# Optimization experiments

Measured on AMD Instinct MI355X. Metric: run time of the kernel, lower is better.

## Reference

```python
import jax, jax.numpy as jnp
import numpy as np

B, S, H = 8, 2048, 1024   # batch, seq, hidden_size
E = 4                     # num_experts (world_size=1 -> all local)
C = 1024                  # kv_cache_size (cache_decrement=0 -> uniform pyramid)
R = 4                     # LoRA rank
ALPHA = 1.0
TOP_K = 2
TEMP = 1.0
KEEP = C // 2             # pyramid compressor keeps top-half by importance


def _lora(z, A, Bm):
    # LoRALayer: (z @ A) @ B scaled by alpha/rank
    return (z @ A) @ Bm * (ALPHA / A.shape[-1])


def setup_inputs() -> dict:
    key = jax.random.key(0)
    ks = jax.random.split(key, 24)
    w = lambda k, shp: jax.random.normal(k, shp, jnp.float32) * 0.02
    return {
        'x': jax.random.normal(ks[0], (B, S, H), jnp.float32),
        'query': jax.random.normal(ks[1], (B, S, H), jnp.float32),
        'Wg': w(ks[2], (H, E)), 'bg': jnp.zeros((E,), jnp.float32),
        'Wq': w(ks[3], (H, H)), 'bq': jnp.zeros((H,), jnp.float32),
        'Wk': w(ks[4], (H, H)), 'bk': jnp.zeros((H,), jnp.float32),
        'Aq': w(ks[5], (H, R)), 'Bq': w(ks[6], (R, H)),
        'Ak': w(ks[7], (H, R)), 'Bk': w(ks[8], (R, H)),
        'We': w(ks[9], (E, H, H)), 'be': jnp.zeros((E, H), jnp.float32),
        'Ae': w(ks[10], (E, H, R)), 'Be': w(ks[11], (E, R, H)),
        'Av': w(ks[12], (E, H, R)), 'Bv': w(ks[13], (E, R, H)),
        'cache_keys': jax.random.normal(ks[14], (E, C, H), jnp.float32),
        'cache_values': jax.random.normal(ks[15], (E, C, H), jnp.float32),
        'cache_imp': jax.random.uniform(ks[16], (E, C), jnp.float32),
    }


def reference(x, query, Wg, bg, Wq, bq, Wk, bk, Aq, Bq, Ak, Bk,
              We, be, Ae, Be, Av, Bv, cache_keys, cache_values, cache_imp):
    # ---- AdaptiveRouter: softmax gate, top-2 renormalized, load-balance loss ----
    probs = jax.nn.softmax((x @ Wg + bg) / TEMP, axis=-1)             # [B,S,E]
    tw, ti = jax.lax.top_k(probs, TOP_K)                              # [B,S,K]
    twn = tw / tw.sum(-1, keepdims=True)
    onehot = jax.nn.one_hot(ti, E, dtype=x.dtype)                     # [B,S,K,E]
    routing = jnp.einsum('bsk,bske->bse', twn, onehot)                # [B,S,E]
    lb_loss = E * jnp.sum(probs.mean((0, 1)) * onehot.mean((0, 1, 2)))

    # ---- compute_token_importance (query provided): LoRA-augmented q/k attention ----
    q = query @ Wq + bq + _lora(query, Aq, Bq)
    k = x @ Wk + bk + _lora(x, Ak, Bk)
    att = jax.nn.softmax(jnp.einsum('bqh,bkh->bqk', q, k) / np.sqrt(H).astype(np.float32), axis=-1)
    importance = att.sum(axis=1)                                      # [B,S] column sums

    # ---- per-expert LoRA forward + pyramid-compressed cache read ----
    def expert_fn(We_i, be_i, Ae_i, Be_i, Av_i, Bv_i, cv_i, ci_i):
        eo = x @ We_i + be_i + _lora(x, Ae_i, Be_i)                   # [B,S,H]
        idx = jax.lax.top_k(ci_i, KEEP)[1]                            # keep top-half by importance
        vals = cv_i[idx]                                              # [KEEP,H] irregular gather
        vals = vals + _lora(vals, Av_i, Bv_i)                         # value LoRA on compressed cache
        return eo + jax.lax.stop_gradient(vals.mean(0))               # cached values are detached

    outs = jax.vmap(expert_fn)(We, be, Ae, Be, Av, Bv, cache_values, cache_imp)  # [E,B,S,H]
    expert_output = jnp.einsum('ebsh,bse->bsh', outs, routing)

    # ---- cache update at ptr=0 (detached buffer mutation -> returned new state) ----
    sg = jax.lax.stop_gradient
    new_keys = cache_keys.at[:, 0].set(jnp.broadcast_to(sg(x.mean((0, 1))), (E, H)))
    new_values = cache_values.at[:, 0].set(sg(outs.mean((1, 2))))
    new_imp = cache_imp.at[:, 0].set(sg(importance.mean()))
    return expert_output, lb_loss, new_keys, new_values, new_imp
```

## Files before the change

kernel.cpp:

```cpp
#include <hip/hip_runtime.h>

constexpr int kH    = 1024;
constexpr int kNT   = 16384;
constexpr int kE    = 4;
constexpr int kC    = 1024;
constexpr int kR    = 4;
constexpr int kKeep = 512;
constexpr float kLoraScale = 0.25f;
constexpr int kCapTiles = 136;
constexpr int kCapRows  = kCapTiles * 128;
constexpr int kNB      = kNT / 256;

constexpr size_t WS_RW     = 0;
constexpr size_t WS_G      = 65536;
constexpr size_t WS_XSUM   = 393216;
constexpr size_t WS_SHADOW = 394240;
constexpr size_t WS_TU     = 394752;
constexpr size_t WS_VBAR   = 394784;
constexpr size_t WS_FX     = 398880;
constexpr size_t WS_NEWV0  = 402976;
constexpr size_t WS_MSK    = 407072;
constexpr size_t WS_GBASE  = 411168;
constexpr size_t WS_BHIST  = 411176;
constexpr size_t WS_BOFF   = 411560;
constexpr size_t WS_RTPID  = 411944;
constexpr size_t WS_TPID   = 412088;
constexpr size_t WS_GRO    = 428472;
constexpr size_t WS_PERM   = 444856;
constexpr size_t WS_WCAT   = 462264;
constexpr size_t WS_AEXT   = 482744;
constexpr size_t WS_AEXTG  = 744888;
constexpr size_t WS_BEXT   = 1023416;
constexpr size_t WS_WET    = 1039800;
constexpr size_t WS_XG     = 3136952;

constexpr size_t OUT_LB = 16777216;
constexpr size_t OUT_NK = 16777217;

typedef __attribute__((ext_vector_type(8))) short bf16x8;
typedef __attribute__((ext_vector_type(4))) float f32x4;

__device__ __forceinline__ float wred(float v) {
#pragma unroll
  for (int off = 32; off; off >>= 1) v += __shfl_xor(v, off);
  return v;
}

__device__ __forceinline__ ushort f2bf(float f) {
  unsigned int u = __float_as_uint(f);
  u += 0x7FFFu + ((u >> 16) & 1u);
  return (ushort)(u >> 16);
}

__device__ __forceinline__ void gload16(const ushort* g, ushort* l) {
  __builtin_amdgcn_global_load_lds(
      (const __attribute__((address_space(1))) unsigned int*)g,
      (__attribute__((address_space(3))) unsigned int*)l, 16, 0, 0);
}

__device__ __forceinline__ int pid_a(int pid) { return pid < 3 ? 0 : (pid < 5 ? 1 : 2); }
__device__ __forceinline__ int pid_b(int pid) { return pid < 3 ? pid + 1 : (pid < 5 ? pid - 1 : 3); }

__global__ __launch_bounds__(256) void wcat_k(const float* __restrict__ Wg,
                                              const float* __restrict__ Ae,
                                              float* __restrict__ wcat) {
  const int idx = blockIdx.x * 256 + threadIdx.x;
  const int c = idx >> 10, k = idx & 1023;
  float v;
  if (c < 4) v = Wg[(size_t)k * 4 + c];
  else {
    const int e = (c - 4) >> 2, r = (c - 4) & 3;
    v = Ae[((size_t)e * kH + k) * kR + r];
  }
  wcat[(size_t)c * kH + k] = v;
}

__global__ __launch_bounds__(256) void router_gemm_k(
    const float* __restrict__ x, const float* __restrict__ wcat,
    float* __restrict__ G) {
  __shared__ float xs_l[128][64];
  __shared__ float wt_l[20][64];
  const int tid = threadIdx.x;
  const int t0 = blockIdx.x * 128;
  const int tok = tid & 127, half = tid >> 7, cb = half * 10;
  float acc[10] = {};
  for (int kc = 0; kc < 16; ++kc) {
#pragma unroll
    for (int i = 0; i < 8; ++i) {
      const int idx = tid + i * 256;
      const int stok = idx >> 4, sslot = idx & 15;
      const float4 v =
          *(const float4*)(x + (size_t)(t0 + stok) * kH + kc * 64 + sslot * 4);
      *(float4*)&xs_l[stok][((sslot + stok) & 15) * 4] = v;
    }
    for (int idx = tid; idx < 320; idx += 256) {
      const int c = idx >> 4, slot = idx & 15;
      *(float4*)&wt_l[c][slot * 4] =
          *(const float4*)(wcat + (size_t)c * kH + kc * 64 + slot * 4);
    }
    __syncthreads();
#pragma unroll
    for (int k4 = 0; k4 < 16; ++k4) {
      const float4 xv = *(const float4*)&xs_l[tok][((k4 + tok) & 15) * 4];
#pragma unroll
      for (int j = 0; j < 10; ++j) {
        const float4 wv = *(const float4*)&wt_l[cb + j][k4 * 4];
        acc[j] += xv.x * wv.x + xv.y * wv.y + xv.z * wv.z + xv.w * wv.w;
      }
    }
    __syncthreads();
  }
#pragma unroll
  for (int j = 0; j < 10; ++j)
    G[(size_t)(cb + j) * kNT + t0 + tok] = acc[j];
}

__global__ __launch_bounds__(256) void router_fin_k(
    const float* __restrict__ G, const float* __restrict__ bg,
    float* __restrict__ rw, float* __restrict__ shadow,
    int* __restrict__ tpid, int* __restrict__ bhist,
    ushort* __restrict__ aext) {
  __shared__ float swacc[8];
  __shared__ int ihist[6];
  const int tid = threadIdx.x;
  const int t = blockIdx.x * 256 + tid;
  const int lane = tid & 63;
  if (tid < 8) swacc[tid] = 0.f;
  if (tid < 6) ihist[tid] = 0;
  __syncthreads();
  float lg[kE];
#pragma unroll
  for (int e = 0; e < kE; ++e) lg[e] = G[(size_t)e * kNT + t] + bg[e];
  float la[kE][kR];
#pragma unroll
  for (int e = 0; e < kE; ++e)
#pragma unroll
    for (int r = 0; r < kR; ++r)
      la[e][r] = G[(size_t)(4 + e * 4 + r) * kNT + t];
  const float mx = fmaxf(fmaxf(lg[0], lg[1]), fmaxf(lg[2], lg[3]));
  float ex[kE], se = 0.f;
#pragma unroll
  for (int e = 0; e < kE; ++e) { ex[e] = __expf(lg[e] - mx); se += ex[e]; }
  float pr[kE];
#pragma unroll
  for (int e = 0; e < kE; ++e) pr[e] = ex[e] / se;
  int e1 = 0;
#pragma unroll
  for (int e = 1; e < kE; ++e) if (pr[e] > pr[e1]) e1 = e;
  int e2 = (e1 == 0) ? 1 : 0;
#pragma unroll
  for (int e = 0; e < kE; ++e) if (e != e1 && pr[e] > pr[e2]) e2 = e;
  const float s2 = pr[e1] + pr[e2];
  float rwv[kE] = {0.f, 0.f, 0.f, 0.f};
  rwv[e1] = pr[e1] / s2; rwv[e2] = pr[e2] / s2;
  *(float4*)(rw + (size_t)t * kE) = make_float4(rwv[0], rwv[1], rwv[2], rwv[3]);
  const int lo = min(e1, e2), hi = max(e1, e2);
  const int pid = (lo == 0) ? hi - 1 : ((lo == 1) ? hi + 1 : 5);
  tpid[t] = pid;
  __align__(16) ushort o[32];
#pragma unroll
  for (int e = 0; e < kE; ++e) o[e] = f2bf(rwv[e]);
#pragma unroll
  for (int e = 0; e < kE; ++e)
#pragma unroll
    for (int r = 0; r < kR; ++r)
      o[4 + e * 4 + r] = f2bf(kLoraScale * rwv[e] * la[e][r]);
#pragma unroll
  for (int i = 20; i < 32; ++i) o[i] = 0;
#pragma unroll
  for (int q = 0; q < 4; ++q)
    *(float4*)&aext[(size_t)t * 32 + q * 8] = *(float4*)&o[q * 8];
  float vals[8];
#pragma unroll
  for (int e = 0; e < kE; ++e) {
    vals[e] = pr[e];
    vals[4 + e] = ((e == e1) ? 1.f : 0.f) + ((e == e2) ? 1.f : 0.f);
  }
#pragma unroll
  for (int j = 0; j < 8; ++j) {
    vals[j] = wred(vals[j]);
    if (lane == 0) atomicAdd(&swacc[j], vals[j]);
  }
  atomicAdd(&ihist[pid], 1);
  __syncthreads();
  if (tid < 8) atomicAdd(&shadow[(blockIdx.x & 63) * 8 + tid], swacc[tid]);
  if (tid < 6) bhist[blockIdx.x * 6 + tid] = ihist[tid];
}

__global__ __launch_bounds__(256) void colsum_k(const float* __restrict__ x,
                                                float* __restrict__ xsum) {
  const int rg = blockIdx.x, tid = threadIdx.x;
  const float* xp = x + (size_t)rg * 64 * kH + tid * 4;
  float s0 = 0.f, s1 = 0.f, s2 = 0.f, s3 = 0.f;
  for (int r = 0; r < 64; ++r) {
    const float4 v = *(const float4*)(xp + (size_t)r * kH);
    s0 += v.x; s1 += v.y; s2 += v.z; s3 += v.w;
  }
  atomicAdd(&xsum[tid * 4 + 0], s0);
  atomicAdd(&xsum[tid * 4 + 1], s1);
  atomicAdd(&xsum[tid * 4 + 2], s2);
  atomicAdd(&xsum[tid * 4 + 3], s3);
}

__global__ __launch_bounds__(256) void pscan_k(const int* __restrict__ bhist,
                                               int* __restrict__ gbase,
                                               int* __restrict__ boff,
                                               int* __restrict__ rtpid,
                                               int* __restrict__ perm) {
  __shared__ int pcnt_s[6];
  const int tid = threadIdx.x;
  if (tid < 6) {
    int run = 0;
    for (int b = 0; b < kNB; ++b) {
      boff[b * 6 + tid] = run;
      run += bhist[b * 6 + tid];
    }
    pcnt_s[tid] = run;
  }
  __syncthreads();
  if (tid == 0) {
    int base = 0;
    for (int g = 0; g < 6; ++g) {
      gbase[g] = base;
      const int tiles = (pcnt_s[g] + 127) >> 7;
      for (int ti = 0; ti < tiles; ++ti) rtpid[(base >> 7) + ti] = g;
      base += tiles << 7;
    }
    for (int i = base >> 7; i < kCapTiles; ++i) rtpid[i] = -1;
  }
  __syncthreads();
  if (tid < 6) {
    const int gb = gbase[tid];
    for (int b = 0; b < kNB; ++b) boff[b * 6 + tid] += gb;
  }
  for (int i = tid; i < kCapRows; i += 256) perm[i] = -1;
}

__global__ __launch_bounds__(256) void slot_k(const int* __restrict__ tpid,
                                              const int* __restrict__ boff,
                                              int* __restrict__ gro,
                                              int* __restrict__ perm) {
  __shared__ int wcnt[4][6];
  const int tid = threadIdx.x, w = tid >> 6, lane = tid & 63;
  const int t = blockIdx.x * 256 + tid;
  const int pid = tpid[t];
  unsigned long long mymask = 0;
  int cnt[6];
#pragma unroll
  for (int g = 0; g < 6; ++g) {
    const unsigned long long m = __ballot(pid == g);
    cnt[g] = __popcll(m);
    if (g == pid) mymask = m;
  }
  if (lane < 6) wcnt[w][lane] = cnt[lane];
  const int rank_in_wave =
      __popcll(mymask & ((lane == 63) ? 0x7FFFFFFFFFFFFFFFULL
                                      : ((1ULL << lane) - 1ULL)));
  __syncthreads();
  int base = 0;
  for (int w2 = 0; w2 < w; ++w2) base += wcnt[w2][pid];
  const int grow = boff[blockIdx.x * 6 + pid] + base + rank_in_wave;
  gro[t] = grow;
  perm[grow] = t;
}

__global__ __launch_bounds__(256) void xg_k(
    const float* __restrict__ x, const float* __restrict__ rw,
    const int* __restrict__ tpid, const ushort* __restrict__ aext,
    const int* __restrict__ gro, ushort* __restrict__ xg,
    ushort* __restrict__ aextg) {
  const int wave = threadIdx.x >> 6, lane = threadIdx.x & 63;
  const int t = blockIdx.x * 4 + wave;
  const int pid = tpid[t];
  const int grow = gro[t];
  const float wa = rw[(size_t)t * 4 + pid_a(pid)];
  const float wb = rw[(size_t)t * 4 + pid_b(pid)];
#pragma unroll
  for (int q = 0; q < 4; ++q) {
    const int c = q * 256 + lane * 4;
    const float4 v = *(const float4*)(x + (size_t)t * kH + c);
    ushort4 ua, ub;
    ua.x = f2bf(wa * v.x); ua.y = f2bf(wa * v.y);
    ua.z = f2bf(wa * v.z); ua.w = f2bf(wa * v.w);
    ub.x = f2bf(wb * v.x); ub.y = f2bf(wb * v.y);
    ub.z = f2bf(wb * v.z); ub.w = f2bf(wb * v.w);
    *(ushort4*)(xg + (size_t)grow * 2048 + c) = ua;
    *(ushort4*)(xg + (size_t)grow * 2048 + 1024 + c) = ub;
  }
  if (lane < 4)
    *(float4*)&aextg[(size_t)grow * 32 + lane * 8] =
        *(const float4*)&aext[(size_t)t * 32 + lane * 8];
}

__global__ __launch_bounds__(256) void wet_k(const float* __restrict__ We,
                                             ushort* __restrict__ wet) {
  __shared__ ushort tile[64][72];
  const int jb = blockIdx.x, kb = blockIdx.y, e = blockIdx.z;
  const int tid = threadIdx.x;
  const int rr = tid >> 4, cq = tid & 15;
#pragma unroll
  for (int p = 0; p < 4; ++p) {
    const int k = kb * 64 + p * 16 + rr;
    const float4 v = *(const float4*)&We[((size_t)e * kH + k) * kH + jb * 64 + cq * 4];
    tile[p * 16 + rr][cq * 4 + 0] = f2bf(v.x);
    tile[p * 16 + rr][cq * 4 + 1] = f2bf(v.y);
    tile[p * 16 + rr][cq * 4 + 2] = f2bf(v.z);
    tile[p * 16 + rr][cq * 4 + 3] = f2bf(v.w);
  }
  __syncthreads();
#pragma unroll
  for (int p = 0; p < 4; ++p) {
    const int j = jb * 64 + p * 16 + rr;
    ushort4 u;
    u.x = tile[cq * 4 + 0][p * 16 + rr];
    u.y = tile[cq * 4 + 1][p * 16 + rr];
    u.z = tile[cq * 4 + 2][p * 16 + rr];
    u.w = tile[cq * 4 + 3][p * 16 + rr];
    *(ushort4*)&wet[((size_t)e * kH + j) * kH + kb * 64 + cq * 4] = u;
  }
}

__global__ __launch_bounds__(256) void keep_k(const float* __restrict__ ci,
                                              float* __restrict__ msk) {
  __shared__ float imp[kC];
  const int e = blockIdx.x, part = blockIdx.y;
  const int c = part * 256 + threadIdx.x;
  for (int i = threadIdx.x; i < kC; i += 256) imp[i] = ci[(size_t)e * kC + i];
  __syncthreads();
  const float v = imp[c];
  int rank = 0;
  for (int c2 = 0; c2 < kC; ++c2) {
    const float v2 = imp[c2];
    rank += (v2 > v) || (v2 == v && c2 < c);
  }
  msk[(size_t)e * kC + c] = (rank < kKeep) ? 1.0f : 0.0f;
}

__global__ __launch_bounds__(256) void vbar_acc_k(const float* __restrict__ cv,
                                                  const float* __restrict__ msk,
                                                  float* __restrict__ vbar) {
  const int e = blockIdx.x, rc = blockIdx.y;
  const int tid = threadIdx.x;
  const float* base = cv + (size_t)e * kC * kH + (size_t)rc * 32 * kH + tid * 4;
  const float* m = msk + (size_t)e * kC + rc * 32;
  float s0 = 0.f, s1 = 0.f, s2 = 0.f, s3 = 0.f;
#pragma unroll 8
  for (int r = 0; r < 32; ++r) {
    const float mr = m[r];
    const float4 v = *(const float4*)(base + (size_t)r * kH);
    s0 += mr * v.x; s1 += mr * v.y; s2 += mr * v.z; s3 += mr * v.w;
  }
  const float sc = 1.0f / kKeep;
  atomicAdd(&vbar[(size_t)e * kH + tid * 4 + 0], s0 * sc);
  atomicAdd(&vbar[(size_t)e * kH + tid * 4 + 1], s1 * sc);
  atomicAdd(&vbar[(size_t)e * kH + tid * 4 + 2], s2 * sc);
  atomicAdd(&vbar[(size_t)e * kH + tid * 4 + 3], s3 * sc);
}

__global__ __launch_bounds__(256) void tu_k(const float* __restrict__ vbar,
                                            const float* __restrict__ xsum,
                                            const float* __restrict__ Av,
                                            const float* __restrict__ Ae,
                                            float* __restrict__ tu) {
  __shared__ float red[256];
  const int e = blockIdx.x, tid = threadIdx.x;
  float p[8] = {};
#pragma unroll
  for (int q = 0; q < 4; ++q) {
    const int h = tid * 4 + q;
    const float vb = vbar[(size_t)e * kH + h];
    const float xm = xsum[h] * (1.0f / kNT);
    const float4 av = *(const float4*)(Av + ((size_t)e * kH + h) * kR);
    const float4 ae = *(const float4*)(Ae + ((size_t)e * kH + h) * kR);
    p[0] += vb * av.x; p[1] += vb * av.y; p[2] += vb * av.z; p[3] += vb * av.w;
    p[4] += xm * ae.x; p[5] += xm * ae.y; p[6] += xm * ae.z; p[7] += xm * ae.w;
  }
#pragma unroll
  for (int j = 0; j < 8; ++j) {
    red[tid] = p[j]; __syncthreads();
    for (int s2 = 128; s2; s2 >>= 1) {
      if (tid < s2) red[tid] += red[tid + s2];
      __syncthreads();
    }
    if (tid == 0) tu[e * 8 + j] = red[0];
    __syncthreads();
  }
}

__global__ __launch_bounds__(256) void fx_acc_k(const float* __restrict__ We,
                                                const float* __restrict__ xsum,
                                                float* __restrict__ fx) {
  const int e = blockIdx.x, kc = blockIdx.y;
  const int tid = threadIdx.x;
  const float* Wb = We + (size_t)e * kH * kH + (size_t)kc * 64 * kH + tid * 4;
  const float* xs = xsum + kc * 64;
  float s0 = 0.f, s1 = 0.f, s2 = 0.f, s3 = 0.f;
#pragma unroll 8
  for (int k = 0; k < 64; ++k) {
    const float xm = xs[k] * (1.0f / kNT);
    const float4 v = *(const float4*)(Wb + (size_t)k * kH);
    s0 += xm * v.x; s1 += xm * v.y; s2 += xm * v.z; s3 += xm * v.w;
  }
  atomicAdd(&fx[(size_t)e * kH + tid * 4 + 0], s0);
  atomicAdd(&fx[(size_t)e * kH + tid * 4 + 1], s1);
  atomicAdd(&fx[(size_t)e * kH + tid * 4 + 2], s2);
  atomicAdd(&fx[(size_t)e * kH + tid * 4 + 3], s3);
}

__global__ __launch_bounds__(256) void fin_k(
    const float* __restrict__ be, const float* __restrict__ Bv,
    const float* __restrict__ Bee, const float* __restrict__ vbar,
    const float* __restrict__ fx, const float* __restrict__ tu,
    float* __restrict__ newv0_ws, ushort* __restrict__ bext) {
  const int e = blockIdx.x, tid = threadIdx.x;
  float t_[4], u_[4];
#pragma unroll
  for (int r = 0; r < kR; ++r) { t_[r] = tu[e * 8 + r]; u_[r] = tu[e * 8 + 4 + r]; }
#pragma unroll
  for (int q = 0; q < 4; ++q) {
    const int col = q * 256 + tid;
    float lv = 0.f, le = 0.f;
#pragma unroll
    for (int r = 0; r < kR; ++r) {
      lv += t_[r] * Bv[((size_t)e * kR + r) * kH + col];
      le += u_[r] * Bee[((size_t)e * kR + r) * kH + col];
    }
    const float mv = vbar[(size_t)e * kH + col] + kLoraScale * lv;
    const float bias = be[(size_t)e * kH + col] + mv;
    newv0_ws[(size_t)e * kH + col] = fx[(size_t)e * kH + col] + kLoraScale * le + bias;
    bext[(size_t)col * 32 + e] = f2bf(bias);
#pragma unroll
    for (int r = 0; r < kR; ++r)
      bext[(size_t)col * 32 + 4 + e * 4 + r] =
          f2bf(Bee[((size_t)e * kR + r) * kH + col]);
    if (e == 0)
#pragma unroll
      for (int i = 20; i < 32; ++i) bext[(size_t)col * 32 + i] = 0;
  }
}

__global__ __launch_bounds__(256, 2) void moe_gemm_pair_k(
    const ushort* __restrict__ xg, const ushort* __restrict__ wet,
    const ushort* __restrict__ aextg, const ushort* __restrict__ bext,
    const int* __restrict__ rtpid, const int* __restrict__ perm,
    float* __restrict__ out) {
  const int bid = blockIdx.x;
  const int gid = (bid & 7) * 136 + (bid >> 3);
  const int rt = gid >> 3, ct = gid & 7;
  const int pid = rtpid[rt];
  if (pid < 0) return;
  __shared__ __align__(16) ushort As[2][128 * 32];
  __shared__ __align__(16) ushort Bs[2][128 * 32];
  __shared__ int perm_s[128];
  const int tid = threadIdx.x;
  const int lane = tid & 63, wave = tid >> 6;
  const int wm = wave >> 1, wn = wave & 1;
  const int r0 = rt * 128, c0 = ct * 128;
  const int ea = pid_a(pid), eb = pid_b(pid);
  if (tid < 128) perm_s[tid] = perm[r0 + tid];

  const int srow = lane >> 2;
  const int sslot = lane & 3;

  auto stage = [&](int buf, int kt) {
#pragma unroll
    for (int i = 0; i < 2; ++i) {
      const int j0 = wave * 32 + i * 16;
      const int r = j0 + srow;
      const int slot = sslot ^ ((r >> 1) & 3);
      const ushort* srcA;
      const ushort* srcB;
      if (kt < 64) {
        const int e = (kt < 32) ? ea : eb;
        const int ko = ((kt & 31) * 32) + ((kt < 32) ? 0 : 1024);
        srcA = xg + (size_t)(r0 + r) * 2048 + ko + slot * 8;
        srcB = wet + ((size_t)e * kH + c0 + r) * kH + (kt & 31) * 32 + slot * 8;
      } else {
        srcA = aextg + (size_t)(r0 + r) * 32 + slot * 8;
        srcB = bext + (size_t)(c0 + r) * 32 + slot * 8;
      }
      gload16(srcA, &As[buf][j0 * 32]);
      gload16(srcB, &Bs[buf][j0 * 32]);
    }
  };

  f32x4 acc[4][4] = {};
  stage(0, 0);
  asm volatile("s_waitcnt vmcnt(0)" ::: "memory");
  __syncthreads();

  const int rA = lane & 15;
  const int fslot = lane >> 4;
  int buf = 0;
  for (int kt = 0; kt <= 64; ++kt) {
    if (kt < 64) stage(buf ^ 1, kt + 1);
    bf16x8 a[4], b[4];
#pragma unroll
    for (int m = 0; m < 4; ++m) {
      const int r = wm * 64 + m * 16 + rA;
      const int sl = fslot ^ ((r >> 1) & 3);
      a[m] = *(const bf16x8*)&As[buf][r * 32 + sl * 8];
    }
#pragma unroll
    for (int n = 0; n < 4; ++n) {
      const int r = wn * 64 + n * 16 + rA;
      const int sl = fslot ^ ((r >> 1) & 3);
      b[n] = *(const bf16x8*)&Bs[buf][r * 32 + sl * 8];
    }
#pragma unroll
    for (int m = 0; m < 4; ++m)
#pragma unroll
      for (int n = 0; n < 4; ++n)
        acc[m][n] = __builtin_amdgcn_mfma_f32_16x16x32_bf16(a[m], b[n], acc[m][n], 0, 0, 0);
    if (kt < 64) asm volatile("s_waitcnt vmcnt(0)" ::: "memory");
    __syncthreads();
    buf ^= 1;
  }

#pragma unroll
  for (int m = 0; m < 4; ++m) {
#pragma unroll
    for (int v = 0; v < 4; ++v) {
      const int rl = wm * 64 + m * 16 + (lane >> 4) * 4 + v;
      const int tok = perm_s[rl];
      if (tok >= 0) {
        float* orow = out + (size_t)tok * kH + c0 + wn * 64 + (lane & 15);
#pragma unroll
        for (int n = 0; n < 4; ++n) orow[n * 16] = acc[m][n][v];
      }
    }
  }
}

__global__ __launch_bounds__(256) void copyfix_k(
    const float* __restrict__ ck, const float* __restrict__ cv,
    const float* __restrict__ ci, const float* __restrict__ xsum,
    const float* __restrict__ newv0, const float* __restrict__ shadow,
    float* __restrict__ out) {
  const size_t NK = (size_t)kE * kC * kH;
  const size_t idx = (size_t)blockIdx.x * 256 + threadIdx.x;
  if (idx < NK) {
    const size_t c = (idx >> 10) & (kC - 1), h = idx & (kH - 1);
    out[OUT_NK + idx] = (c == 0) ? xsum[h] * (1.0f / kNT) : ck[idx];
  } else if (idx < 2 * NK) {
    const size_t j = idx - NK;
    const size_t e = j >> 20, c = (j >> 10) & (kC - 1), h = j & (kH - 1);
    out[OUT_NK + idx] = (c == 0) ? newv0[e * kH + h] : cv[j];
  } else if (idx < 2 * NK + (size_t)kE * kC) {
    const size_t j = idx - 2 * NK;
    out[OUT_NK + idx] = ((j & (kC - 1)) == 0) ? 1.0f : ci[j];
  } else if (idx == 2 * NK + (size_t)kE * kC) {
    float lb = 0.f;
#pragma unroll
    for (int e = 0; e < kE; ++e) {
      float ps = 0.f, cn = 0.f;
      for (int s2 = 0; s2 < 64; ++s2) {
        ps += shadow[s2 * 8 + e];
        cn += shadow[s2 * 8 + 4 + e];
      }
      lb += (ps * (1.0f / kNT)) * (cn * (1.0f / (kNT * 2.0f)));
    }
    out[OUT_LB] = kE * lb;
  }
}

extern "C" void kernel_launch(void* const* d_in, const int* in_sizes, int n_in,
                              void* d_out, int out_size, void* d_ws, size_t ws_size,
                              hipStream_t stream) {
  const float* x   = (const float*)d_in[0];
  const float* Wg  = (const float*)d_in[2];
  const float* bg  = (const float*)d_in[3];
  const float* We  = (const float*)d_in[12];
  const float* be  = (const float*)d_in[13];
  const float* Ae  = (const float*)d_in[14];
  const float* Bee = (const float*)d_in[15];
  const float* Av  = (const float*)d_in[16];
  const float* Bv  = (const float*)d_in[17];
  const float* ck  = (const float*)d_in[18];
  const float* cv  = (const float*)d_in[19];
  const float* ci  = (const float*)d_in[20];
  float* ws  = (float*)d_ws;
  float* out = (float*)d_out;

  int* tpid  = (int*)(ws + WS_TPID);
  int* bhist = (int*)(ws + WS_BHIST);
  int* boff  = (int*)(ws + WS_BOFF);
  int* gbase = (int*)(ws + WS_GBASE);
  int* rtpid = (int*)(ws + WS_RTPID);
  int* gro   = (int*)(ws + WS_GRO);
  int* perm  = (int*)(ws + WS_PERM);
  ushort* aext  = (ushort*)(ws + WS_AEXT);
  ushort* aextg = (ushort*)(ws + WS_AEXTG);
  ushort* bext  = (ushort*)(ws + WS_BEXT);
  ushort* wet   = (ushort*)(ws + WS_WET);
  ushort* xg    = (ushort*)(ws + WS_XG);

  hipMemsetAsync(ws + WS_XSUM, 0, 9760 * sizeof(float), stream);
  colsum_k<<<256, 256, 0, stream>>>(x, ws + WS_XSUM);
  wcat_k<<<80, 256, 0, stream>>>(Wg, Ae, ws + WS_WCAT);
  router_gemm_k<<<kNT / 128, 256, 0, stream>>>(x, ws + WS_WCAT, ws + WS_G);
  router_fin_k<<<kNB, 256, 0, stream>>>(ws + WS_G, bg, ws + WS_RW,
                                        ws + WS_SHADOW, tpid, bhist, aext);
  pscan_k<<<1, 256, 0, stream>>>(bhist, gbase, boff, rtpid, perm);
  slot_k<<<kNB, 256, 0, stream>>>(tpid, boff, gro, perm);
  xg_k<<<kNT / 4, 256, 0, stream>>>(x, ws + WS_RW, tpid, aext, gro, xg, aextg);
  wet_k<<<dim3(16, 16, 4), 256, 0, stream>>>(We, wet);
  keep_k<<<dim3(kE, 4), 256, 0, stream>>>(ci, ws + WS_MSK);
  vbar_acc_k<<<dim3(kE, 32), 256, 0, stream>>>(cv, ws + WS_MSK, ws + WS_VBAR);
  fx_acc_k<<<dim3(kE, 16), 256, 0, stream>>>(We, ws + WS_XSUM, ws + WS_FX);
  tu_k<<<kE, 256, 0, stream>>>(ws + WS_VBAR, ws + WS_XSUM, Av, Ae, ws + WS_TU);
  fin_k<<<kE, 256, 0, stream>>>(be, Bv, Bee, ws + WS_VBAR, ws + WS_FX,
                                ws + WS_TU, ws + WS_NEWV0, bext);
  moe_gemm_pair_k<<<kCapTiles * 8, 256, 0, stream>>>(
      xg, wet, aextg, bext, rtpid, perm, out);
  copyfix_k<<<32785, 256, 0, stream>>>(ck, cv, ci, ws + WS_XSUM, ws + WS_NEWV0,
                                       ws + WS_SHADOW, out);
}
```

Before: 373.4 us.

## Triple-buffer MoE GEMM prefetch and merge small setup kernels

The MoE GEMM goes from double to triple buffering in LDS. It prefetches two k-tiles ahead, waits with a partial vmcnt instead of draining all loads, and raises the occupancy hint to 3 blocks per CU. Separately, wcat_k and keep_k are merged into one prep_k launch, and tu_k and fin_k are merged into tufin_k, which cuts kernel launches. The extra LDS buffer raises shared memory per block, and the fixed vmcnt(4) count assumes exactly four outstanding loads per stage.

After: 381.2 us. +2.1%, slower.

```diff
diff --git a/kernel.cpp b/kernel.cpp
--- a/kernel.cpp
+++ b/kernel.cpp
@@ -61,18 +61,36 @@
 __device__ __forceinline__ int pid_a(int pid) { return pid < 3 ? 0 : (pid < 5 ? 1 : 2); }
 __device__ __forceinline__ int pid_b(int pid) { return pid < 3 ? pid + 1 : (pid < 5 ? pid - 1 : 3); }
 
-__global__ __launch_bounds__(256) void wcat_k(const float* __restrict__ Wg,
+__global__ __launch_bounds__(256) void prep_k(const float* __restrict__ Wg,
                                               const float* __restrict__ Ae,
-                                              float* __restrict__ wcat) {
-  const int idx = blockIdx.x * 256 + threadIdx.x;
-  const int c = idx >> 10, k = idx & 1023;
-  float v;
-  if (c < 4) v = Wg[(size_t)k * 4 + c];
-  else {
-    const int e = (c - 4) >> 2, r = (c - 4) & 3;
-    v = Ae[((size_t)e * kH + k) * kR + r];
-  }
-  wcat[(size_t)c * kH + k] = v;
+                                              const float* __restrict__ ci,
+                                              float* __restrict__ wcat,
+                                              float* __restrict__ msk) {
+  __shared__ float imp[kC];
+  const int b = blockIdx.x, tid = threadIdx.x;
+  if (b < 80) {
+    const int idx = b * 256 + tid;
+    const int c = idx >> 10, k = idx & 1023;
+    float v;
+    if (c < 4) v = Wg[(size_t)k * 4 + c];
+    else {
+      const int e = (c - 4) >> 2, r = (c - 4) & 3;
+      v = Ae[((size_t)e * kH + k) * kR + r];
+    }
+    wcat[(size_t)c * kH + k] = v;
+  } else {
+    const int e = (b - 80) >> 2, part = (b - 80) & 3;
+    const int c = part * 256 + tid;
+    for (int i = tid; i < kC; i += 256) imp[i] = ci[(size_t)e * kC + i];
+    __syncthreads();
+    const float v = imp[c];
+    int rank = 0;
+    for (int c2 = 0; c2 < kC; ++c2) {
+      const float v2 = imp[c2];
+      rank += (v2 > v) || (v2 == v && c2 < c);
+    }
+    msk[(size_t)e * kC + c] = (rank < kKeep) ? 1.0f : 0.0f;
+  }
 }
 
 __global__ __launch_bounds__(256) void router_gemm_k(
@@ -320,22 +338,6 @@
   }
 }
 
-__global__ __launch_bounds__(256) void keep_k(const float* __restrict__ ci,
-                                              float* __restrict__ msk) {
-  __shared__ float imp[kC];
-  const int e = blockIdx.x, part = blockIdx.y;
-  const int c = part * 256 + threadIdx.x;
-  for (int i = threadIdx.x; i < kC; i += 256) imp[i] = ci[(size_t)e * kC + i];
-  __syncthreads();
-  const float v = imp[c];
-  int rank = 0;
-  for (int c2 = 0; c2 < kC; ++c2) {
-    const float v2 = imp[c2];
-    rank += (v2 > v) || (v2 == v && c2 < c);
-  }
-  msk[(size_t)e * kC + c] = (rank < kKeep) ? 1.0f : 0.0f;
-}
-
 __global__ __launch_bounds__(256) void vbar_acc_k(const float* __restrict__ cv,
                                                   const float* __restrict__ msk,
                                                   float* __restrict__ vbar) {
@@ -357,36 +359,6 @@
   atomicAdd(&vbar[(size_t)e * kH + tid * 4 + 3], s3 * sc);
 }
 
-__global__ __launch_bounds__(256) void tu_k(const float* __restrict__ vbar,
-                                            const float* __restrict__ xsum,
-                                            const float* __restrict__ Av,
-                                            const float* __restrict__ Ae,
-                                            float* __restrict__ tu) {
-  __shared__ float red[256];
-  const int e = blockIdx.x, tid = threadIdx.x;
-  float p[8] = {};
-#pragma unroll
-  for (int q = 0; q < 4; ++q) {
-    const int h = tid * 4 + q;
-    const float vb = vbar[(size_t)e * kH + h];
-    const float xm = xsum[h] * (1.0f / kNT);
-    const float4 av = *(const float4*)(Av + ((size_t)e * kH + h) * kR);
-    const float4 ae = *(const float4*)(Ae + ((size_t)e * kH + h) * kR);
-    p[0] += vb * av.x; p[1] += vb * av.y; p[2] += vb * av.z; p[3] += vb * av.w;
-    p[4] += xm * ae.x; p[5] += xm * ae.y; p[6] += xm * ae.z; p[7] += xm * ae.w;
-  }
-#pragma unroll
-  for (int j = 0; j < 8; ++j) {
-    red[tid] = p[j]; __syncthreads();
-    for (int s2 = 128; s2; s2 >>= 1) {
-      if (tid < s2) red[tid] += red[tid + s2];
-      __syncthreads();
-    }
-    if (tid == 0) tu[e * 8 + j] = red[0];
-    __syncthreads();
-  }
-}
-
 __global__ __launch_bounds__(256) void fx_acc_k(const float* __restrict__ We,
                                                 const float* __restrict__ xsum,
                                                 float* __restrict__ fx) {
@@ -407,15 +379,39 @@
   atomicAdd(&fx[(size_t)e * kH + tid * 4 + 3], s3);
 }
 
-__global__ __launch_bounds__(256) void fin_k(
+__global__ __launch_bounds__(256) void tufin_k(
+    const float* __restrict__ vbar, const float* __restrict__ xsum,
+    const float* __restrict__ Av, const float* __restrict__ Ae,
     const float* __restrict__ be, const float* __restrict__ Bv,
-    const float* __restrict__ Bee, const float* __restrict__ vbar,
-    const float* __restrict__ fx, const float* __restrict__ tu,
+    const float* __restrict__ Bee, const float* __restrict__ fx,
     float* __restrict__ newv0_ws, ushort* __restrict__ bext) {
+  __shared__ float red[256];
+  __shared__ float tus[8];
   const int e = blockIdx.x, tid = threadIdx.x;
+  float p[8] = {};
+#pragma unroll
+  for (int q = 0; q < 4; ++q) {
+    const int h = tid * 4 + q;
+    const float vb = vbar[(size_t)e * kH + h];
+    const float xm = xsum[h] * (1.0f / kNT);
+    const float4 av = *(const float4*)(Av + ((size_t)e * kH + h) * kR);
+    const float4 ae = *(const float4*)(Ae + ((size_t)e * kH + h) * kR);
+    p[0] += vb * av.x; p[1] += vb * av.y; p[2] += vb * av.z; p[3] += vb * av.w;
+    p[4] += xm * ae.x; p[5] += xm * ae.y; p[6] += xm * ae.z; p[7] += xm * ae.w;
+  }
+#pragma unroll
+  for (int j = 0; j < 8; ++j) {
+    red[tid] = p[j]; __syncthreads();
+    for (int s2 = 128; s2; s2 >>= 1) {
+      if (tid < s2) red[tid] += red[tid + s2];
+      __syncthreads();
+    }
+    if (tid == 0) tus[j] = red[0];
+    __syncthreads();
+  }
   float t_[4], u_[4];
 #pragma unroll
-  for (int r = 0; r < kR; ++r) { t_[r] = tu[e * 8 + r]; u_[r] = tu[e * 8 + 4 + r]; }
+  for (int r = 0; r < kR; ++r) { t_[r] = tus[r]; u_[r] = tus[4 + r]; }
 #pragma unroll
   for (int q = 0; q < 4; ++q) {
     const int col = q * 256 + tid;
@@ -439,7 +435,7 @@
   }
 }
 
-__global__ __launch_bounds__(256, 2) void moe_gemm_pair_k(
+__global__ __launch_bounds__(256, 3) void moe_gemm_pair_k(
     const ushort* __restrict__ xg, const ushort* __restrict__ wet,
     const ushort* __restrict__ aextg, const ushort* __restrict__ bext,
     const int* __restrict__ rtpid, const int* __restrict__ perm,
@@ -449,8 +445,8 @@
   const int rt = gid >> 3, ct = gid & 7;
   const int pid = rtpid[rt];
   if (pid < 0) return;
-  __shared__ __align__(16) ushort As[2][128 * 32];
-  __shared__ __align__(16) ushort Bs[2][128 * 32];
+  __shared__ __align__(16) ushort As[3][128 * 32];
+  __shared__ __align__(16) ushort Bs[3][128 * 32];
   __shared__ int perm_s[128];
   const int tid = threadIdx.x;
   const int lane = tid & 63, wave = tid >> 6;
@@ -486,35 +482,45 @@
 
   f32x4 acc[4][4] = {};
   stage(0, 0);
-  asm volatile("s_waitcnt vmcnt(0)" ::: "memory");
-  __syncthreads();
+  stage(1, 1);
+  asm volatile("s_waitcnt vmcnt(4)" ::: "memory");
+  __builtin_amdgcn_sched_barrier(0);
+  __builtin_amdgcn_s_barrier();
 
   const int rA = lane & 15;
   const int fslot = lane >> 4;
-  int buf = 0;
+  int cur = 0, prev = 2;
   for (int kt = 0; kt <= 64; ++kt) {
-    if (kt < 64) stage(buf ^ 1, kt + 1);
+    if (kt + 2 <= 64) stage(prev, kt + 2);
     bf16x8 a[4], b[4];
 #pragma unroll
     for (int m = 0; m < 4; ++m) {
       const int r = wm * 64 + m * 16 + rA;
       const int sl = fslot ^ ((r >> 1) & 3);
-      a[m] = *(const bf16x8*)&As[buf][r * 32 + sl * 8];
+      a[m] = *(const bf16x8*)&As[cur][r * 32 + sl * 8];
     }
 #pragma unroll
     for (int n = 0; n < 4; ++n) {
       const int r = wn * 64 + n * 16 + rA;
       const int sl = fslot ^ ((r >> 1) & 3);
-      b[n] = *(const bf16x8*)&Bs[buf][r * 32 + sl * 8];
+      b[n] = *(const bf16x8*)&Bs[cur][r * 32 + sl * 8];
     }
 #pragma unroll
     for (int m = 0; m < 4; ++m)
 #pragma unroll
       for (int n = 0; n < 4; ++n)
         acc[m][n] = __builtin_amdgcn_mfma_f32_16x16x32_bf16(a[m], b[n], acc[m][n], 0, 0, 0);
-    if (kt < 64) asm volatile("s_waitcnt vmcnt(0)" ::: "memory");
-    __syncthreads();
-    buf ^= 1;
+    if (kt < 64) {
+      if (kt < 63) {
+        asm volatile("s_waitcnt vmcnt(4)" ::: "memory");
+      } else {
+        asm volatile("s_waitcnt vmcnt(0)" ::: "memory");
+      }
+      __builtin_amdgcn_sched_barrier(0);
+      __builtin_amdgcn_s_barrier();
+    }
+    prev = cur;
+    cur = (cur == 2) ? 0 : cur + 1;
   }
 
 #pragma unroll
@@ -596,8 +602,8 @@
   ushort* xg    = (ushort*)(ws + WS_XG);
 
   hipMemsetAsync(ws + WS_XSUM, 0, 9760 * sizeof(float), stream);
+  prep_k<<<96, 256, 0, stream>>>(Wg, Ae, ci, ws + WS_WCAT, ws + WS_MSK);
   colsum_k<<<256, 256, 0, stream>>>(x, ws + WS_XSUM);
-  wcat_k<<<80, 256, 0, stream>>>(Wg, Ae, ws + WS_WCAT);
   router_gemm_k<<<kNT / 128, 256, 0, stream>>>(x, ws + WS_WCAT, ws + WS_G);
   router_fin_k<<<kNB, 256, 0, stream>>>(ws + WS_G, bg, ws + WS_RW,
                                         ws + WS_SHADOW, tpid, bhist, aext);
@@ -605,12 +611,10 @@
   slot_k<<<kNB, 256, 0, stream>>>(tpid, boff, gro, perm);
   xg_k<<<kNT / 4, 256, 0, stream>>>(x, ws + WS_RW, tpid, aext, gro, xg, aextg);
   wet_k<<<dim3(16, 16, 4), 256, 0, stream>>>(We, wet);
-  keep_k<<<dim3(kE, 4), 256, 0, stream>>>(ci, ws + WS_MSK);
   vbar_acc_k<<<dim3(kE, 32), 256, 0, stream>>>(cv, ws + WS_MSK, ws + WS_VBAR);
   fx_acc_k<<<dim3(kE, 16), 256, 0, stream>>>(We, ws + WS_XSUM, ws + WS_FX);
-  tu_k<<<kE, 256, 0, stream>>>(ws + WS_VBAR, ws + WS_XSUM, Av, Ae, ws + WS_TU);
-  fin_k<<<kE, 256, 0, stream>>>(be, Bv, Bee, ws + WS_VBAR, ws + WS_FX,
-                                ws + WS_TU, ws + WS_NEWV0, bext);
+  tufin_k<<<kE, 256, 0, stream>>>(ws + WS_VBAR, ws + WS_XSUM, Av, Ae, be, Bv,
+                                  Bee, ws + WS_FX, ws + WS_NEWV0, bext);
   moe_gemm_pair_k<<<kCapTiles * 8, 256, 0, stream>>>(
       xg, wet, aextg, bext, rtpid, perm, out);
   copyfix_k<<<32785, 256, 0, stream>>>(ck, cv, ci, ws + WS_XSUM, ws + WS_NEWV0,
```
